# Performance work log

Hardware: AMD Instinct MI355X
Metric: run time of the kernel (lower is better)

The kernel has to match this reference:

```python
import jax, jax.numpy as jnp
import numpy as np

E = 2048      # embedding_size
H = 16        # num_heads
D = 128       # head_dim
G = 4         # gqa_factor
KH = H // G   # kv heads
F = 8192      # up_proj_size
B, S = 2, 2048


def _layer_norm(x, g, b, eps=1e-5):
    mu = jnp.mean(x, axis=-1, keepdims=True)
    var = jnp.mean(jnp.square(x - mu), axis=-1, keepdims=True)
    return (x - mu) * jax.lax.rsqrt(var + eps) * g + b


def setup_inputs() -> dict:
    key = jax.random.key(0)
    ks = jax.random.split(key, 16)
    std = 0.02
    inp = {
        'x': jax.random.normal(ks[0], (B, S, E), dtype=jnp.float32),
        'ln1_g': jnp.ones((E,), jnp.float32),
        'ln1_b': jnp.zeros((E,), jnp.float32),
        'wq': jax.random.normal(ks[1], (E, H * D), jnp.float32) * std,
        'bq': jnp.zeros((H * D,), jnp.float32),
        'wk': jax.random.normal(ks[2], (E, KH * D), jnp.float32) * std,
        'bk': jnp.zeros((KH * D,), jnp.float32),
        'wv': jax.random.normal(ks[3], (E, KH * D), jnp.float32) * std,
        'bv': jnp.zeros((KH * D,), jnp.float32),
        'wo': jax.random.normal(ks[4], (H * D, E), jnp.float32) * std,
        'bo': jnp.zeros((E,), jnp.float32),
        'ln2_g': jnp.ones((E,), jnp.float32),
        'ln2_b': jnp.zeros((E,), jnp.float32),
        'wu': jax.random.normal(ks[5], (E, F), jnp.float32) * std,
        'bu': jnp.zeros((F,), jnp.float32),
        'wd': jax.random.normal(ks[6], (F, E), jnp.float32) * std,
        'bd': jnp.zeros((E,), jnp.float32),
    }
    return inp


def _block(x, ln1_g, ln1_b, wq, bq, wk, bk, wv, bv, wo, bo, ln2_g, ln2_b, wu, bu, wd, bd):
    b, s, e = x.shape
    # attention sub-block (use_cache=False, train_mode=False -> no dropout)
    x1 = _layer_norm(x, ln1_g, ln1_b)
    q = (x1 @ wq + bq).reshape(b, s, H, D).transpose(0, 2, 1, 3)       # (B,H,S,D)
    q = q.reshape(b, KH, G, s, D)                                       # (B,KH,G,S,D)
    k = (x1 @ wk + bk).reshape(b, s, KH, D).transpose(0, 2, 1, 3)      # (B,KH,S,D)
    v = (x1 @ wv + bv).reshape(b, s, KH, D).transpose(0, 2, 1, 3)      # (B,KH,S,D)
    scores = jnp.einsum('bkgsd,bktd->bkgst', q, k) / np.sqrt(D).astype(np.float32)
    causal = jnp.tril(jnp.ones((s, s), dtype=bool))                     # True = keep
    scores = jnp.where(causal, scores, -jnp.inf)
    att = jax.nn.softmax(scores, axis=-1)
    o = jnp.einsum('bkgst,bktd->bkgsd', att, v)                         # (B,KH,G,S,D)
    o = o.reshape(b, H, s, D).transpose(0, 2, 1, 3).reshape(b, s, H * D)
    x = x + (o @ wo + bo)
    # MLP sub-block
    x2 = _layer_norm(x, ln2_g, ln2_b)
    h = jax.nn.gelu(x2 @ wu + bu, approximate=False)
    x = x + (h @ wd + bd)
    return x


def reference(x, ln1_g, ln1_b, wq, bq, wk, bk, wv, bv, wo, bo, ln2_g, ln2_b, wu, bu, wd, bd):
    return _block(x, ln1_g, ln1_b, wq, bq, wk, bk, wv, bv, wo, bo, ln2_g, ln2_b, wu, bu, wd, bd)
```

## Files before the change

kernel.cpp:

```cpp
#include <hip/hip_runtime.h>
#include <hip/hip_bf16.h>
#include <cstdint>
#include <math.h>

typedef unsigned short u16;
using f32x4   = __attribute__((ext_vector_type(4))) float;
using short8  = __attribute__((ext_vector_type(8))) short;
using short4v = __attribute__((ext_vector_type(4))) short;

#define DEV static __device__ __forceinline__

DEV u16 f2bf(float f) {
  union { float f; unsigned u; } v; v.f = f;
  unsigned r = v.u + 0x7fffu + ((v.u >> 16) & 1u);
  return (u16)(r >> 16);
}

DEV f32x4 mfma_bf16(short8 a, short8 b, f32x4 c) {
  return __builtin_amdgcn_mfma_f32_16x16x32_bf16(a, b, c, 0, 0, 0);
}

DEV void gload16(const void* g, void* l) {
  __builtin_amdgcn_global_load_lds((const __attribute__((address_space(1))) void*)g,
                                   (__attribute__((address_space(3))) void*)l,
                                   16, 0, 0);
}

__global__ __launch_bounds__(256) void transpose_cvt(
    const float* __restrict__ in, u16* __restrict__ out, int K, int N)
{
  __shared__ float tile[32][33];
  const int n0 = blockIdx.x * 32, k0 = blockIdx.y * 32;
  const int c = threadIdx.x & 31, r = threadIdx.x >> 5;
#pragma unroll
  for (int i = 0; i < 4; i++) {
    const int row = r + i * 8;
    tile[row][c] = in[(size_t)(k0 + row) * N + n0 + c];
  }
  __syncthreads();
#pragma unroll
  for (int i = 0; i < 4; i++) {
    const int row = r + i * 8;
    out[(size_t)(n0 + row) * K + k0 + c] = f2bf(tile[c][row]);
  }
}

__global__ __launch_bounds__(256) void ln_kernel(
    const float* __restrict__ x, const float* __restrict__ g,
    const float* __restrict__ bt, u16* __restrict__ out)
{
  __shared__ float red1[4], red2[4];
  const int row = blockIdx.x;
  const int t = threadIdx.x;
  const int lane = t & 63, w = t >> 6;
  const float* xr = x + (size_t)row * 2048 + t * 8;
  float v[8];
  {
    const float4* p4 = (const float4*)xr;
    float4 a = p4[0], b = p4[1];
    v[0] = a.x; v[1] = a.y; v[2] = a.z; v[3] = a.w;
    v[4] = b.x; v[5] = b.y; v[6] = b.z; v[7] = b.w;
  }
  float s = 0.f;
#pragma unroll
  for (int j = 0; j < 8; j++) s += v[j];
#pragma unroll
  for (int m = 1; m < 64; m <<= 1) s += __shfl_xor(s, m);
  if (lane == 0) red1[w] = s;
  __syncthreads();
  const float mu = (red1[0] + red1[1] + red1[2] + red1[3]) * (1.f / 2048.f);
  float q = 0.f;
#pragma unroll
  for (int j = 0; j < 8; j++) { v[j] -= mu; q += v[j] * v[j]; }
#pragma unroll
  for (int m = 1; m < 64; m <<= 1) q += __shfl_xor(q, m);
  if (lane == 0) red2[w] = q;
  __syncthreads();
  const float rstd = rsqrtf((red2[0] + red2[1] + red2[2] + red2[3]) * (1.f / 2048.f) + 1e-5f);
  const float4* g4 = (const float4*)(g + t * 8);
  const float4* b4 = (const float4*)(bt + t * 8);
  float4 ga = g4[0], gb = g4[1], ba = b4[0], bb = b4[1];
  float gg[8] = {ga.x, ga.y, ga.z, ga.w, gb.x, gb.y, gb.z, gb.w};
  float bbv[8] = {ba.x, ba.y, ba.z, ba.w, bb.x, bb.y, bb.z, bb.w};
  short8 o;
#pragma unroll
  for (int j = 0; j < 8; j++) o[j] = (short)f2bf(v[j] * rstd * gg[j] + bbv[j]);
  *(short8*)&out[(size_t)row * 2048 + t * 8] = o;
}

template<int MODE, int N, int K>
__global__ void __launch_bounds__(256) gemm_bt(
    const u16* __restrict__ A, const u16* __restrict__ Bt,
    const float* __restrict__ bias, const float* __restrict__ resid,
    u16* __restrict__ out_bf, float* __restrict__ out_f)
{
  __shared__ u16 As[128 * 64];
  __shared__ u16 Bs[128 * 64];
  const int m0 = blockIdx.y * 128;
  const int n0 = blockIdx.x * 128;
  const int tid = threadIdx.x;
  const int lane = tid & 63, w = tid >> 6;
  const int wm = w >> 1, wn = w & 1;
  const int z = lane >> 4, l15 = lane & 15;

  f32x4 acc[4][4];
#pragma unroll
  for (int m = 0; m < 4; m++)
#pragma unroll
    for (int n = 0; n < 4; n++)
#pragma unroll
      for (int i = 0; i < 4; i++) acc[m][n][i] = 0.f;

  for (int k0 = 0; k0 < K; k0 += 64) {
#pragma unroll
    for (int j = 0; j < 4; j++) {
      const int seg = w * 4 + j;
      const int c = seg * 64 + lane;
      const int r = c >> 3;
      const int cc = (c & 7) ^ (r & 7);
      gload16(A + (size_t)(m0 + r) * K + k0 + cc * 8, &As[seg * 512]);
    }
#pragma unroll
    for (int j = 0; j < 4; j++) {
      const int seg = w * 4 + j;
      const int c = seg * 64 + lane;
      const int r = c >> 3;
      const int cc = (c & 7) ^ (r & 7);
      gload16(Bt + (size_t)(n0 + r) * K + k0 + cc * 8, &Bs[seg * 512]);
    }
    asm volatile("s_waitcnt vmcnt(0)" ::: "memory");
    __syncthreads();

#pragma unroll
    for (int kk = 0; kk < 2; kk++) {
      short8 af[4], bfr[4];
#pragma unroll
      for (int m = 0; m < 4; m++) {
        const int row = wm * 64 + m * 16 + l15;
        const int off = row * 64 + ((kk * 32 + z * 8) ^ ((row & 7) << 3));
        af[m] = *(const short8*)&As[off];
      }
#pragma unroll
      for (int n = 0; n < 4; n++) {
        const int row = wn * 64 + n * 16 + l15;
        const int off = row * 64 + ((kk * 32 + z * 8) ^ ((row & 7) << 3));
        bfr[n] = *(const short8*)&Bs[off];
      }
#pragma unroll
      for (int m = 0; m < 4; m++)
#pragma unroll
        for (int n = 0; n < 4; n++)
          acc[m][n] = mfma_bf16(af[m], bfr[n], acc[m][n]);
    }
    __syncthreads();
  }

#pragma unroll
  for (int m = 0; m < 4; m++) {
    const int row0 = m0 + wm * 64 + m * 16 + z * 4;
#pragma unroll
    for (int n = 0; n < 4; n++) {
      const int col = n0 + wn * 64 + n * 16 + l15;
      f32x4 v = acc[m][n];
      const float bb = bias[col];
      if constexpr (MODE == 0) {
#pragma unroll
        for (int i = 0; i < 4; i++)
          out_bf[(size_t)(row0 + i) * N + col] = f2bf((v[i] + bb) * 0.08838834764831845f);
      } else if constexpr (MODE == 1) {
#pragma unroll
        for (int i = 0; i < 4; i++)
          out_bf[(size_t)(row0 + i) * N + col] = f2bf(v[i] + bb);
      } else if constexpr (MODE == 2) {
        const int bidx = row0 >> 11, sidx = row0 & 2047;
        const int kh = col >> 7, d = col & 127;
        short4v p;
#pragma unroll
        for (int i = 0; i < 4; i++) p[i] = (short)f2bf(v[i] + bb);
        *(short4v*)&out_bf[(size_t)((bidx * 4 + kh) * 128 + d) * 2048 + sidx] = p;
      } else if constexpr (MODE == 3) {
#pragma unroll
        for (int i = 0; i < 4; i++) {
          const size_t idx = (size_t)(row0 + i) * N + col;
          out_f[idx] = v[i] + bb + resid[idx];
        }
      } else if constexpr (MODE == 4) {
#pragma unroll
        for (int i = 0; i < 4; i++) {
          const float xx = v[i] + bb;
          out_bf[(size_t)(row0 + i) * N + col] =
              f2bf(0.5f * xx * (1.f + erff(xx * 0.70710678118654752f)));
        }
      } else {
#pragma unroll
        for (int i = 0; i < 4; i++) {
          const size_t idx = (size_t)(row0 + i) * N + col;
          out_f[idx] = v[i] + bb + out_f[idx];
        }
      }
    }
  }
}

__global__ void __launch_bounds__(256) attn_kernel(
    const u16* __restrict__ qb, const u16* __restrict__ kb,
    const u16* __restrict__ vt, u16* __restrict__ ob)
{
  __shared__ u16 Kt[2][64 * 128];
  __shared__ u16 Vs[2][128 * 64];
  __shared__ u16 Pl[4 * 32 * 64];

  const int idx = blockIdx.x;
  const int xcd = idx & 7;
  const int u = (idx >> 3) & 31;
  const int half = idx >> 8;
  const int bh = xcd * 4 + (u & 3);
  const int qh = u >> 2;
  const int qt = half ? (15 - qh) : qh;

  const int b = bh >> 4, h = bh & 15, kh = h >> 2;
  const int q0 = qt * 128;
  const int tid = threadIdx.x, lane = tid & 63, w = tid >> 6;
  const int z = lane >> 4, l15 = lane & 15;
  const int qw0 = q0 + w * 32;
  const int ksw = (l15 & 7) << 3;

  short8 qf[2][4];
#pragma unroll
  for (int m = 0; m < 2; m++)
#pragma unroll
    for (int kk = 0; kk < 4; kk++)
      qf[m][kk] = *(const short8*)&qb[(size_t)(b * 2048 + qw0 + m * 16 + l15) * 2048 +
                                      h * 128 + kk * 32 + z * 8];

  f32x4 oacc[2][8];
#pragma unroll
  for (int m = 0; m < 2; m++)
#pragma unroll
    for (int n = 0; n < 8; n++)
#pragma unroll
      for (int i = 0; i < 4; i++) oacc[m][n][i] = 0.f;
  float mst[2][4], lst[2][4];
#pragma unroll
  for (int m = 0; m < 2; m++)
#pragma unroll
    for (int i = 0; i < 4; i++) { mst[m][i] = -1e30f; lst[m][i] = 0.f; }

  auto STAGE = [&](int tt, int bufsel) {
    const int kv0s = tt * 64;
#pragma unroll
    for (int j = 0; j < 4; j++) {
      const int seg = w * 4 + j;
      const int c = seg * 64 + lane;
      const int r = c >> 4;
      const int cc = (c & 15) ^ (r & 7);
      gload16(kb + (size_t)(b * 2048 + kv0s + r) * 512 + kh * 128 + cc * 8,
              &Kt[bufsel][seg * 512]);
    }
#pragma unroll
    for (int j = 0; j < 4; j++) {
      const int seg = w * 4 + j;
      const int c = seg * 64 + lane;
      const int d = c >> 3;
      const int cc = (c & 7) ^ (d & 7);
      gload16(vt + (size_t)((b * 4 + kh) * 128 + d) * 2048 + kv0s + cc * 8,
              &Vs[bufsel][seg * 512]);
    }
  };

  const int ntiles = q0 / 64 + 2;

  STAGE(0, 0);
  asm volatile("s_waitcnt vmcnt(0)" ::: "memory");
  __syncthreads();

  for (int t = 0; t < ntiles; t++) {
    const int cur = t & 1;
    if (t + 1 < ntiles) STAGE(t + 1, cur ^ 1);

    const int kv0 = t * 64;
    if (kv0 <= qw0 + 31) {
      f32x4 sf[2][4];
#pragma unroll
      for (int m = 0; m < 2; m++)
#pragma unroll
        for (int n = 0; n < 4; n++)
#pragma unroll
          for (int i = 0; i < 4; i++) sf[m][n][i] = 0.f;

      __builtin_amdgcn_s_setprio(1);
#pragma unroll
      for (int kk = 0; kk < 4; kk++) {
        short8 kfr[4];
#pragma unroll
        for (int n = 0; n < 4; n++) {
          const int row = n * 16 + l15;
          kfr[n] = *(const short8*)&Kt[cur][row * 128 + ((kk * 32 + z * 8) ^ ksw)];
        }
#pragma unroll
        for (int m = 0; m < 2; m++)
#pragma unroll
          for (int n = 0; n < 4; n++)
            sf[m][n] = mfma_bf16(qf[m][kk], kfr[n], sf[m][n]);
      }
      __builtin_amdgcn_s_setprio(0);

      u16* Pw = &Pl[w * 2048];
      const bool edge = (kv0 + 63 > qw0);
#pragma unroll
      for (int m = 0; m < 2; m++) {
#pragma unroll
        for (int i = 0; i < 4; i++) {
          const int rq = qw0 + m * 16 + z * 4 + i;
          if (edge) {
#pragma unroll
            for (int n = 0; n < 4; n++)
              if (kv0 + n * 16 + l15 > rq) sf[m][n][i] = -1e30f;
          }
          float mx = fmaxf(fmaxf(sf[m][0][i], sf[m][1][i]), fmaxf(sf[m][2][i], sf[m][3][i]));
          mx = fmaxf(mx, __shfl_xor(mx, 1));
          mx = fmaxf(mx, __shfl_xor(mx, 2));
          mx = fmaxf(mx, __shfl_xor(mx, 4));
          mx = fmaxf(mx, __shfl_xor(mx, 8));
          const bool grow = mx > mst[m][i];
          const float mn = grow ? mx : mst[m][i];
          float rs = 0.f;
#pragma unroll
          for (int n = 0; n < 4; n++) {
            const float p = __expf(sf[m][n][i] - mn);
            sf[m][n][i] = p;
            rs += p;
          }
          rs += __shfl_xor(rs, 1);
          rs += __shfl_xor(rs, 2);
          rs += __shfl_xor(rs, 4);
          rs += __shfl_xor(rs, 8);
          if (grow) {
            const float al = __expf(mst[m][i] - mx);
            mst[m][i] = mx;
            lst[m][i] = lst[m][i] * al + rs;
#pragma unroll
            for (int n = 0; n < 8; n++) oacc[m][n][i] *= al;
          } else {
            lst[m][i] += rs;
          }
          const int prow = m * 16 + z * 4 + i;
          const int psw = ((z * 4 + i) & 7) << 3;
#pragma unroll
          for (int n = 0; n < 4; n++)
            Pw[prow * 64 + ((n * 16 + l15) ^ psw)] = f2bf(sf[m][n][i]);
        }
      }

      __builtin_amdgcn_s_setprio(1);
#pragma unroll
      for (int kk = 0; kk < 2; kk++) {
        short8 af[2], vf[8];
#pragma unroll
        for (int m = 0; m < 2; m++) {
          const int row = m * 16 + l15;
          af[m] = *(const short8*)&Pw[row * 64 + ((kk * 32 + z * 8) ^ ksw)];
        }
#pragma unroll
        for (int n = 0; n < 8; n++) {
          const int row = n * 16 + l15;
          vf[n] = *(const short8*)&Vs[cur][row * 64 + ((kk * 32 + z * 8) ^ ksw)];
        }
#pragma unroll
        for (int m = 0; m < 2; m++)
#pragma unroll
          for (int n = 0; n < 8; n++)
            oacc[m][n] = mfma_bf16(af[m], vf[n], oacc[m][n]);
      }
      __builtin_amdgcn_s_setprio(0);
    }

    asm volatile("s_waitcnt vmcnt(0)" ::: "memory");
    __syncthreads();
  }

#pragma unroll
  for (int m = 0; m < 2; m++)
#pragma unroll
    for (int i = 0; i < 4; i++) {
      const float inv = 1.0f / lst[m][i];
      const int rq = qw0 + m * 16 + z * 4 + i;
      u16* orow = &ob[(size_t)(b * 2048 + rq) * 2048 + h * 128];
#pragma unroll
      for (int n = 0; n < 8; n++)
        orow[n * 16 + l15] = f2bf(oacc[m][n][i] * inv);
    }
}

extern "C" void kernel_launch(void* const* d_in, const int* in_sizes, int n_in,
                              void* d_out, int out_size, void* d_ws, size_t ws_size,
                              hipStream_t stream) {
  (void)in_sizes; (void)n_in; (void)out_size; (void)ws_size;
  const float* x     = (const float*)d_in[0];
  const float* ln1_g = (const float*)d_in[1];
  const float* ln1_b = (const float*)d_in[2];
  const float* wq    = (const float*)d_in[3];
  const float* bq    = (const float*)d_in[4];
  const float* wk    = (const float*)d_in[5];
  const float* bk    = (const float*)d_in[6];
  const float* wv    = (const float*)d_in[7];
  const float* bv    = (const float*)d_in[8];
  const float* wo    = (const float*)d_in[9];
  const float* bo    = (const float*)d_in[10];
  const float* ln2_g = (const float*)d_in[11];
  const float* ln2_b = (const float*)d_in[12];
  const float* wu    = (const float*)d_in[13];
  const float* bu    = (const float*)d_in[14];
  const float* wd    = (const float*)d_in[15];
  const float* bd    = (const float*)d_in[16];
  float* out = (float*)d_out;

  char* p = (char*)d_ws;
  u16* wqT = (u16*)p; p += (size_t)2048 * 2048 * 2;
  u16* wkT = (u16*)p; p += (size_t)512 * 2048 * 2;
  u16* wvT = (u16*)p; p += (size_t)512 * 2048 * 2;
  u16* woT = (u16*)p; p += (size_t)2048 * 2048 * 2;
  u16* wuT = (u16*)p; p += (size_t)8192 * 2048 * 2;
  u16* wdT = (u16*)p; p += (size_t)2048 * 8192 * 2;
  u16* x1  = (u16*)p; p += (size_t)4096 * 2048 * 2;
  u16* qbuf= (u16*)p; p += (size_t)4096 * 2048 * 2;
  u16* kbuf= (u16*)p; p += (size_t)4096 * 512 * 2;
  u16* vtb = (u16*)p; p += (size_t)4096 * 512 * 2;
  u16* hb  = (u16*)p; p += (size_t)4096 * 8192 * 2;
  u16* ob  = x1;
  u16* x2  = qbuf;

  transpose_cvt<<<dim3(64, 64),  256, 0, stream>>>(wq, wqT, 2048, 2048);
  transpose_cvt<<<dim3(16, 64),  256, 0, stream>>>(wk, wkT, 2048, 512);
  transpose_cvt<<<dim3(16, 64),  256, 0, stream>>>(wv, wvT, 2048, 512);
  transpose_cvt<<<dim3(64, 64),  256, 0, stream>>>(wo, woT, 2048, 2048);
  transpose_cvt<<<dim3(256, 64), 256, 0, stream>>>(wu, wuT, 2048, 8192);
  transpose_cvt<<<dim3(64, 256), 256, 0, stream>>>(wd, wdT, 8192, 2048);

  ln_kernel<<<4096, 256, 0, stream>>>(x, ln1_g, ln1_b, x1);

  gemm_bt<0, 2048, 2048><<<dim3(16, 32), 256, 0, stream>>>(x1, wqT, bq, nullptr, qbuf, nullptr);
  gemm_bt<1, 512,  2048><<<dim3(4, 32),  256, 0, stream>>>(x1, wkT, bk, nullptr, kbuf, nullptr);
  gemm_bt<2, 512,  2048><<<dim3(4, 32),  256, 0, stream>>>(x1, wvT, bv, nullptr, vtb,  nullptr);

  attn_kernel<<<512, 256, 0, stream>>>(qbuf, kbuf, vtb, ob);

  gemm_bt<3, 2048, 2048><<<dim3(16, 32), 256, 0, stream>>>(ob, woT, bo, x, nullptr, out);

  ln_kernel<<<4096, 256, 0, stream>>>(out, ln2_g, ln2_b, x2);

  gemm_bt<4, 8192, 2048><<<dim3(64, 32), 256, 0, stream>>>(x2, wuT, bu, nullptr, hb, nullptr);
  gemm_bt<5, 2048, 8192><<<dim3(16, 32), 256, 0, stream>>>(hb, wdT, bd, nullptr, nullptr, out);
}
```

Before: 805.6 us.

## Add 256-wide GEMM kernel with swizzled LDS and XCD-aware block mapping

Adds a new gemm256 kernel with 512 threads, 128x256 or 256x256 tiles, direct global-to-LDS loads into an XOR-swizzled double buffer split into K halves, explicit vmcnt waits for pipelining, and s_setprio around the MFMA blocks. Blocks are remapped so consecutive workgroups on the same XCD share tiles. The Q, O-projection, up-projection and down-projection GEMMs use it, while the K and V projections stay on the old kernel with a trimmed signature. The goal is more reuse per tile and better overlap of loads with MFMA, at the cost of higher register and LDS pressure and lower occupancy.

```diff
diff --git a/kernel.cpp b/kernel.cpp
--- a/kernel.cpp
+++ b/kernel.cpp
@@ -91,8 +91,8 @@
 template<int MODE, int N, int K>
 __global__ void __launch_bounds__(256) gemm_bt(
     const u16* __restrict__ A, const u16* __restrict__ Bt,
-    const float* __restrict__ bias, const float* __restrict__ resid,
-    u16* __restrict__ out_bf, float* __restrict__ out_f)
+    const float* __restrict__ bias,
+    u16* __restrict__ out_bf)
 {
   __shared__ u16 As[128 * 64];
   __shared__ u16 Bs[128 * 64];
@@ -163,21 +163,118 @@
       const int col = n0 + wn * 64 + n * 16 + l15;
       f32x4 v = acc[m][n];
       const float bb = bias[col];
-      if constexpr (MODE == 0) {
-#pragma unroll
-        for (int i = 0; i < 4; i++)
-          out_bf[(size_t)(row0 + i) * N + col] = f2bf((v[i] + bb) * 0.08838834764831845f);
-      } else if constexpr (MODE == 1) {
+      if constexpr (MODE == 1) {
 #pragma unroll
         for (int i = 0; i < 4; i++)
           out_bf[(size_t)(row0 + i) * N + col] = f2bf(v[i] + bb);
-      } else if constexpr (MODE == 2) {
+      } else {
         const int bidx = row0 >> 11, sidx = row0 & 2047;
         const int kh = col >> 7, d = col & 127;
         short4v p;
 #pragma unroll
         for (int i = 0; i < 4; i++) p[i] = (short)f2bf(v[i] + bb);
         *(short4v*)&out_bf[(size_t)((bidx * 4 + kh) * 128 + d) * 2048 + sidx] = p;
+      }
+    }
+  }
+}
+
+template<int MODE, int BM, int N, int K>
+__global__ void __launch_bounds__(512) gemm256(
+    const u16* __restrict__ A, const u16* __restrict__ Bt,
+    const float* __restrict__ bias, const float* __restrict__ resid,
+    u16* __restrict__ out_bf, float* __restrict__ out_f)
+{
+  constexpr int BN = 256;
+  constexpr int MREP = BM / 32;
+  constexpr int LA = BM / 128;
+  constexpr int L = LA + 2;
+  constexpr int NT = K / 64;
+  constexpr int NWG = (4096 / BM) * (N / BN);
+  constexpr int CPX = NWG / 8;
+
+  __shared__ u16 Al[2][2][BM * 32];
+  __shared__ u16 Bl[2][2][BN * 32];
+
+  const int bid = blockIdx.x;
+  const int wg = (bid & 7) * CPX + (bid >> 3);
+  const int bm = wg / (N / BN), bn = wg % (N / BN);
+  const int m0 = bm * BM, n0 = bn * BN;
+  const int tid = threadIdx.x, lane = tid & 63, w = tid >> 6;
+  const int wm = w >> 2, wn = w & 3;
+  const int z = lane >> 4, l15 = lane & 15;
+
+  f32x4 acc[MREP][4];
+#pragma unroll
+  for (int m = 0; m < MREP; m++)
+#pragma unroll
+    for (int n = 0; n < 4; n++)
+#pragma unroll
+      for (int i = 0; i < 4; i++) acc[m][n][i] = 0.f;
+
+  auto stage = [&](int tt, int kh) {
+    const int buf = tt & 1;
+    const int kc = tt * 64 + kh * 32;
+#pragma unroll
+    for (int j = 0; j < LA; j++) {
+      const int gl = (w * LA + j) * 64 + lane;
+      const int r = gl >> 2, gg = gl & 3;
+      const int cg = gg ^ ((r >> 1) & 3);
+      gload16(A + (size_t)(m0 + r) * K + kc + cg * 8, &Al[buf][kh][(w * LA + j) * 512]);
+    }
+#pragma unroll
+    for (int j = 0; j < 2; j++) {
+      const int gl = (w * 2 + j) * 64 + lane;
+      const int r = gl >> 2, gg = gl & 3;
+      const int cg = gg ^ ((r >> 1) & 3);
+      gload16(Bt + (size_t)(n0 + r) * K + kc + cg * 8, &Bl[buf][kh][(w * 2 + j) * 512]);
+    }
+  };
+
+  stage(0, 0); stage(0, 1); stage(1, 0); stage(1, 1);
+
+  for (int t = 0; t < NT; t++) {
+    const int cb = t & 1;
+#pragma unroll
+    for (int kh = 0; kh < 2; kh++) {
+      if constexpr (L == 4) asm volatile("s_waitcnt vmcnt(4)" ::: "memory");
+      else                  asm volatile("s_waitcnt vmcnt(3)" ::: "memory");
+      __builtin_amdgcn_s_barrier();
+      if (t + 1 < NT) stage(t + 1, kh);
+
+      short8 af[MREP], bf[4];
+#pragma unroll
+      for (int m = 0; m < MREP; m++) {
+        const int r = wm * (BM / 2) + m * 16 + l15;
+        af[m] = *(const short8*)&Al[cb][kh][r * 32 + ((z ^ ((r >> 1) & 3)) * 8)];
+      }
+#pragma unroll
+      for (int n = 0; n < 4; n++) {
+        const int r = wn * 64 + n * 16 + l15;
+        bf[n] = *(const short8*)&Bl[cb][kh][r * 32 + ((z ^ ((r >> 1) & 3)) * 8)];
+      }
+      __builtin_amdgcn_s_setprio(1);
+#pragma unroll
+      for (int m = 0; m < MREP; m++)
+#pragma unroll
+        for (int n = 0; n < 4; n++)
+          acc[m][n] = mfma_bf16(af[m], bf[n], acc[m][n]);
+      __builtin_amdgcn_s_setprio(0);
+    }
+  }
+
+#pragma unroll
+  for (int m = 0; m < MREP; m++) {
+    const int row0 = m0 + wm * (BM / 2) + m * 16 + z * 4;
+#pragma unroll
+    for (int n = 0; n < 4; n++) {
+      const int col = n0 + wn * 64 + n * 16 + l15;
+      f32x4 v = acc[m][n];
+      const float bb = bias[col];
+      if constexpr (MODE == 0) {
+#pragma unroll
+        for (int i = 0; i < 4; i++)
+          out_bf[(size_t)(row0 + i) * N + col] = f2bf((v[i] + bb) * 0.08838834764831845f);
       } else if constexpr (MODE == 3) {
 #pragma unroll
         for (int i = 0; i < 4; i++) {
@@ -439,16 +536,16 @@
 
   ln_kernel<<<4096, 256, 0, stream>>>(x, ln1_g, ln1_b, x1);
 
-  gemm_bt<0, 2048, 2048><<<dim3(16, 32), 256, 0, stream>>>(x1, wqT, bq, nullptr, qbuf, nullptr);
-  gemm_bt<1, 512,  2048><<<dim3(4, 32),  256, 0, stream>>>(x1, wkT, bk, nullptr, kbuf, nullptr);
-  gemm_bt<2, 512,  2048><<<dim3(4, 32),  256, 0, stream>>>(x1, wvT, bv, nullptr, vtb,  nullptr);
+  gemm256<0, 128, 2048, 2048><<<256, 512, 0, stream>>>(x1, wqT, bq, nullptr, qbuf, nullptr);
+  gemm_bt<1, 512, 2048><<<dim3(4, 32), 256, 0, stream>>>(x1, wkT, bk, kbuf);
+  gemm_bt<2, 512, 2048><<<dim3(4, 32), 256, 0, stream>>>(x1, wvT, bv, vtb);
 
   attn_kernel<<<512, 256, 0, stream>>>(qbuf, kbuf, vtb, ob);
 
-  gemm_bt<3, 2048, 2048><<<dim3(16, 32), 256, 0, stream>>>(ob, woT, bo, x, nullptr, out);
+  gemm256<3, 128, 2048, 2048><<<256, 512, 0, stream>>>(ob, woT, bo, x, nullptr, out);
 
   ln_kernel<<<4096, 256, 0, stream>>>(out, ln2_g, ln2_b, x2);
 
-  gemm_bt<4, 8192, 2048><<<dim3(64, 32), 256, 0, stream>>>(x2, wuT, bu, nullptr, hb, nullptr);
-  gemm_bt<5, 2048, 8192><<<dim3(16, 32), 256, 0, stream>>>(hb, wdT, bd, nullptr, nullptr, out);
-}
+  gemm256<4, 256, 8192, 2048><<<512, 512, 0, stream>>>(x2, wuT, bu, nullptr, hb, nullptr);
+  gemm256<5, 128, 2048, 8192><<<256, 512, 0, stream>>>(hb, wdT, bd, nullptr, nullptr, out);
+}
```

Result: slower. 836.9 us (+3.9%).

## Double-buffer GEMM loads, fuse QKV projections, and remap tiles across XCDs

Applied to the files above, without the earlier changes.

Replaces the single-buffered GEMM with a double-buffered version. The next K-tile's global-to-LDS loads are issued while the current tile runs through MFMA, which is meant to hide load latency behind compute. The Q, K and V projections are merged into one 3072-wide GEMM whose epilogue routes columns to the three outputs; this relies on the transposed weights lying contiguously in the workspace. The grid is now 1D and remapped so each XCD works on contiguous M or N stripes for better L2 reuse. MFMA sections are also wrapped in s_setprio, at the cost of twice the LDS use per block, which may lower occupancy.

```diff
diff --git a/kernel.cpp b/kernel.cpp
--- a/kernel.cpp
+++ b/kernel.cpp
@@ -88,16 +88,30 @@
   *(short8*)&out[(size_t)row * 2048 + t * 8] = o;
 }
 
-template<int MODE, int N, int K>
-__global__ void __launch_bounds__(256) gemm_bt(
+template<int MODE, int N, int K, int STRIPE_N>
+__global__ void __launch_bounds__(256) gemm_db(
     const u16* __restrict__ A, const u16* __restrict__ Bt,
-    const float* __restrict__ bias, const float* __restrict__ resid,
-    u16* __restrict__ out_bf, float* __restrict__ out_f)
+    const float* __restrict__ b0, const float* __restrict__ b1,
+    const float* __restrict__ b2, const float* __restrict__ resid,
+    u16* __restrict__ o0, u16* __restrict__ o1, u16* __restrict__ o2,
+    float* __restrict__ of)
 {
-  __shared__ u16 As[128 * 64];
-  __shared__ u16 Bs[128 * 64];
-  const int m0 = blockIdx.y * 128;
-  const int n0 = blockIdx.x * 128;
+  __shared__ u16 As[2][128 * 64];
+  __shared__ u16 Bs[2][128 * 64];
+  constexpr int TN = N / 128;
+  constexpr int NT = K / 64;
+
+  const int bid = blockIdx.x;
+  const int xcd = bid & 7, wl = bid >> 3;
+  int m0, n0;
+  if constexpr (STRIPE_N) {
+    constexpr int NSTR = TN / 8;
+    n0 = (xcd * NSTR + (wl % NSTR)) * 128;
+    m0 = (wl / NSTR) * 128;
+  } else {
+    m0 = (xcd * 4 + (wl & 3)) * 128;
+    n0 = (wl >> 2) * 128;
+  }
   const int tid = threadIdx.x;
   const int lane = tid & 63, w = tid >> 6;
   const int wm = w >> 1, wn = w & 1;
@@ -111,14 +125,14 @@
 #pragma unroll
       for (int i = 0; i < 4; i++) acc[m][n][i] = 0.f;
 
-  for (int k0 = 0; k0 < K; k0 += 64) {
+  auto stage = [&](int k0, int buf) {
 #pragma unroll
     for (int j = 0; j < 4; j++) {
       const int seg = w * 4 + j;
       const int c = seg * 64 + lane;
       const int r = c >> 3;
       const int cc = (c & 7) ^ (r & 7);
-      gload16(A + (size_t)(m0 + r) * K + k0 + cc * 8, &As[seg * 512]);
+      gload16(A + (size_t)(m0 + r) * K + k0 + cc * 8, &As[buf][seg * 512]);
     }
 #pragma unroll
     for (int j = 0; j < 4; j++) {
@@ -126,10 +140,17 @@
       const int c = seg * 64 + lane;
       const int r = c >> 3;
       const int cc = (c & 7) ^ (r & 7);
-      gload16(Bt + (size_t)(n0 + r) * K + k0 + cc * 8, &Bs[seg * 512]);
-    }
-    asm volatile("s_waitcnt vmcnt(0)" ::: "memory");
-    __syncthreads();
+      gload16(Bt + (size_t)(n0 + r) * K + k0 + cc * 8, &Bs[buf][seg * 512]);
+    }
+  };
+
+  stage(0, 0);
+  asm volatile("s_waitcnt vmcnt(0)" ::: "memory");
+  __syncthreads();
+
+  int cur = 0;
+  for (int t = 0; t < NT; t++) {
+    if (t + 1 < NT) stage((t + 1) * 64, cur ^ 1);
 
 #pragma unroll
     for (int kk = 0; kk < 2; kk++) {
@@ -138,21 +159,26 @@
       for (int m = 0; m < 4; m++) {
         const int row = wm * 64 + m * 16 + l15;
         const int off = row * 64 + ((kk * 32 + z * 8) ^ ((row & 7) << 3));
-        af[m] = *(const short8*)&As[off];
+        af[m] = *(const short8*)&As[cur][off];
       }
 #pragma unroll
       for (int n = 0; n < 4; n++) {
         const int row = wn * 64 + n * 16 + l15;
         const int off = row * 64 + ((kk * 32 + z * 8) ^ ((row & 7) << 3));
-        bfr[n] = *(const short8*)&Bs[off];
-      }
+        bfr[n] = *(const short8*)&Bs[cur][off];
+      }
+      __builtin_amdgcn_s_setprio(1);
 #pragma unroll
       for (int m = 0; m < 4; m++)
 #pragma unroll
         for (int n = 0; n < 4; n++)
           acc[m][n] = mfma_bf16(af[m], bfr[n], acc[m][n]);
-    }
+      __builtin_amdgcn_s_setprio(0);
+    }
+
+    asm volatile("s_waitcnt vmcnt(0)" ::: "memory");
     __syncthreads();
+    cur ^= 1;
   }
 
 #pragma unroll
@@ -162,40 +188,50 @@
     for (int n = 0; n < 4; n++) {
       const int col = n0 + wn * 64 + n * 16 + l15;
       f32x4 v = acc[m][n];
-      const float bb = bias[col];
-      if constexpr (MODE == 0) {
-#pragma unroll
-        for (int i = 0; i < 4; i++)
-          out_bf[(size_t)(row0 + i) * N + col] = f2bf((v[i] + bb) * 0.08838834764831845f);
-      } else if constexpr (MODE == 1) {
-#pragma unroll
-        for (int i = 0; i < 4; i++)
-          out_bf[(size_t)(row0 + i) * N + col] = f2bf(v[i] + bb);
-      } else if constexpr (MODE == 2) {
-        const int bidx = row0 >> 11, sidx = row0 & 2047;
-        const int kh = col >> 7, d = col & 127;
-        short4v p;
-#pragma unroll
-        for (int i = 0; i < 4; i++) p[i] = (short)f2bf(v[i] + bb);
-        *(short4v*)&out_bf[(size_t)((bidx * 4 + kh) * 128 + d) * 2048 + sidx] = p;
-      } else if constexpr (MODE == 3) {
-#pragma unroll
-        for (int i = 0; i < 4; i++) {
-          const size_t idx = (size_t)(row0 + i) * N + col;
-          out_f[idx] = v[i] + bb + resid[idx];
-        }
-      } else if constexpr (MODE == 4) {
-#pragma unroll
-        for (int i = 0; i < 4; i++) {
-          const float xx = v[i] + bb;
-          out_bf[(size_t)(row0 + i) * N + col] =
-              f2bf(0.5f * xx * (1.f + erff(xx * 0.70710678118654752f)));
+      if constexpr (MODE == 6) {
+        if (col < 2048) {
+          const float bb = b0[col];
+#pragma unroll
+          for (int i = 0; i < 4; i++)
+            o0[(size_t)(row0 + i) * 2048 + col] = f2bf((v[i] + bb) * 0.08838834764831845f);
+        } else if (col < 2560) {
+          const int ck = col - 2048;
+          const float bb = b1[ck];
+#pragma unroll
+          for (int i = 0; i < 4; i++)
+            o1[(size_t)(row0 + i) * 512 + ck] = f2bf(v[i] + bb);
+        } else {
+          const int cc = col - 2560;
+          const float bb = b2[cc];
+          const int kh = cc >> 7, d = cc & 127;
+          const int bidx = row0 >> 11, sidx = row0 & 2047;
+          u16* vrow = &o2[((size_t)(bidx * 4 + kh) * 128 + d) * 2048 + sidx];
+          short4v pq;
+#pragma unroll
+          for (int i = 0; i < 4; i++) pq[i] = (short)f2bf(v[i] + bb);
+          *(short4v*)vrow = pq;
         }
       } else {
-#pragma unroll
-        for (int i = 0; i < 4; i++) {
-          const size_t idx = (size_t)(row0 + i) * N + col;
-          out_f[idx] = v[i] + bb + out_f[idx];
+        const float bb = b0[col];
+        if constexpr (MODE == 3) {
+#pragma unroll
+          for (int i = 0; i < 4; i++) {
+            const size_t idx = (size_t)(row0 + i) * N + col;
+            of[idx] = v[i] + bb + resid[idx];
+          }
+        } else if constexpr (MODE == 4) {
+#pragma unroll
+          for (int i = 0; i < 4; i++) {
+            const float xx = v[i] + bb;
+            o0[(size_t)(row0 + i) * N + col] =
+                f2bf(0.5f * xx * (1.f + erff(xx * 0.70710678118654752f)));
+          }
+        } else {
+#pragma unroll
+          for (int i = 0; i < 4; i++) {
+            const size_t idx = (size_t)(row0 + i) * N + col;
+            of[idx] = v[i] + bb + of[idx];
+          }
         }
       }
     }
@@ -439,16 +475,18 @@
 
   ln_kernel<<<4096, 256, 0, stream>>>(x, ln1_g, ln1_b, x1);
 
-  gemm_bt<0, 2048, 2048><<<dim3(16, 32), 256, 0, stream>>>(x1, wqT, bq, nullptr, qbuf, nullptr);
-  gemm_bt<1, 512,  2048><<<dim3(4, 32),  256, 0, stream>>>(x1, wkT, bk, nullptr, kbuf, nullptr);
-  gemm_bt<2, 512,  2048><<<dim3(4, 32),  256, 0, stream>>>(x1, wvT, bv, nullptr, vtb,  nullptr);
+  gemm_db<6, 3072, 2048, 0><<<768, 256, 0, stream>>>(
+      x1, wqT, bq, bk, bv, nullptr, qbuf, kbuf, vtb, nullptr);
 
   attn_kernel<<<512, 256, 0, stream>>>(qbuf, kbuf, vtb, ob);
 
-  gemm_bt<3, 2048, 2048><<<dim3(16, 32), 256, 0, stream>>>(ob, woT, bo, x, nullptr, out);
+  gemm_db<3, 2048, 2048, 0><<<512, 256, 0, stream>>>(
+      ob, woT, bo, nullptr, nullptr, x, nullptr, nullptr, nullptr, out);
 
   ln_kernel<<<4096, 256, 0, stream>>>(out, ln2_g, ln2_b, x2);
 
-  gemm_bt<4, 8192, 2048><<<dim3(64, 32), 256, 0, stream>>>(x2, wuT, bu, nullptr, hb, nullptr);
-  gemm_bt<5, 2048, 8192><<<dim3(16, 32), 256, 0, stream>>>(hb, wdT, bd, nullptr, nullptr, out);
-}
+  gemm_db<4, 8192, 2048, 1><<<2048, 256, 0, stream>>>(
+      x2, wuT, bu, nullptr, nullptr, nullptr, hb, nullptr, nullptr, nullptr);
+  gemm_db<5, 2048, 8192, 1><<<512, 256, 0, stream>>>(
+      hb, wdT, bd, nullptr, nullptr, nullptr, nullptr, nullptr, nullptr, out);
+}
```

Measured after the change: 731.1 us. 1.1x faster.
